# Kernel optimization log

Hardware: AMD Instinct MI355X
Metric: run time of the kernel (lower is better)

## Reference

```python
import jax, jax.numpy as jnp
import numpy as np

NBITS = 8
REDUCE = 64
OUT = 512


def setup_inputs() -> dict:
    key = jax.random.key(0)
    ks = jax.random.split(key, 6)
    T, B, C = 512, 16, 512
    ne = 2 ** NBITS
    x = jax.random.normal(ks[0], (T, B, C), dtype=jnp.float32)
    key_in = jax.random.normal(ks[1], (T, B, C), dtype=jnp.float32)  # unused by forward (overwritten)
    # xavier-ish init scales
    map_w = jax.random.normal(ks[2], (NBITS, C), dtype=jnp.float32) * np.sqrt(2.0 / (C + NBITS))
    map_b = jnp.zeros((NBITS,), dtype=jnp.float32)
    pw_w1 = jax.random.normal(ks[3], (REDUCE, C), dtype=jnp.float32) * np.sqrt(2.0 / (C + REDUCE))
    pw_w21 = jax.random.normal(ks[4], (ne, OUT * REDUCE), dtype=jnp.float32) * np.sqrt(2.0 / (ne + OUT * REDUCE))
    pw_w22 = jax.random.normal(ks[5], (ne, OUT * REDUCE), dtype=jnp.float32) * np.sqrt(2.0 / (ne + OUT * REDUCE))
    pw_B = jnp.zeros((1, 1, OUT), dtype=jnp.float32)
    return {"x": x, "key": key_in, "map_w": map_w, "map_b": map_b,
            "pw_w1": pw_w1, "pw_w21": pw_w21, "pw_w22": pw_w22, "pw_B": pw_B}


def reference(x, key, map_w, map_b, pw_w1, pw_w21, pw_w22, pw_B):
    # x: (T,B,C). `key` arg is overwritten by x in the original source.
    T, B, C = x.shape
    nbits = map_w.shape[0]
    out_dim = pw_B.shape[-1]
    reduce_dim = pw_w1.shape[0]

    k = x.reshape(T * B, C) @ map_w.T + map_b          # (T*B, nbits)
    z = jnp.clip(1.2 * jax.nn.sigmoid(k) - 0.1, 0.0, 1.0)  # saturated sigmoid
    code = (z > 0.5).astype(z.dtype)                   # eval: hard binary code

    pows = (2 ** jnp.arange(nbits, dtype=jnp.int32))   # bit_to_int weights
    qz1 = jnp.sum(code.astype(jnp.int32) * pows, axis=-1)          # (T*B,)
    qz2 = jnp.sum((1 - code.astype(jnp.int32)) * pows, axis=-1)    # (T*B,)

    # gather per-token expert rows and synthesize per-token weight matrix
    w2 = (pw_w21[qz1] + pw_w22[qz2]).reshape(T, B, out_dim, reduce_dim)

    # original computes (w2 @ pw_w1) @ x; reassociated as w2 @ (pw_w1 @ x)
    # to avoid materializing the (T,B,out,in) intermediate (same math)
    v = jnp.einsum('ri,tbi->tbr', pw_w1, x)            # (T,B,reduce)
    y = jnp.einsum('tbor,tbr->tbo', w2, v) + pw_B      # (T,B,out)

    loss = jnp.zeros((1,), dtype=x.dtype)
    return (y, loss)
```

## Files before the change

### kernel.cpp

```cpp
#include <hip/hip_runtime.h>

#define NTOK 8192
#define CDIM 512
#define NB   8
#define RD   64
#define OD   512

#define TPB_A 16
#define XPAD  4
#define XROW  (CDIM + XPAD)
#define XROW4 (XROW / 4)

typedef unsigned char u8;

__device__ __forceinline__ float4 f4add(float4 a, float4 b) {
    return make_float4(a.x + b.x, a.y + b.y, a.z + b.z, a.w + b.w);
}
__device__ __forceinline__ float dot4(float4 a, float4 b) {
    return a.x * b.x + a.y * b.y + a.z * b.z + a.w * b.w;
}

__global__ __launch_bounds__(128, 2) void phaseA(
    const float* __restrict__ x, const float* __restrict__ map_w,
    const float* __restrict__ map_b, const float* __restrict__ w1,
    u8* __restrict__ q_out, float* __restrict__ v_out,
    float* __restrict__ loss_out)
{
    const int t    = threadIdx.x;
    const int tok0 = blockIdx.x * TPB_A;
    __shared__ __align__(16) float xs[TPB_A * XROW];

    const float4* xsrc = (const float4*)(x + (size_t)tok0 * CDIM);
    #pragma unroll
    for (int i = t; i < TPB_A * (CDIM / 4); i += 128) {
        int r = i >> 7, c = i & 127;
        *((float4*)(xs + r * XROW) + c) = xsrc[i];
    }
    __syncthreads();

    {
        const int bit = t & 7, tk = t >> 3;
        const float4* m4 = (const float4*)(map_w + (size_t)bit * CDIM);
        const float4* x4 = (const float4*)xs + tk * XROW4;
        double a0 = 0.0, a1 = 0.0;
        for (int j = 0; j < CDIM / 4; ++j) {
            float4 m = m4[j], xv = x4[j];
            a0 += (double)m.x * (double)xv.x + (double)m.y * (double)xv.y;
            a1 += (double)m.z * (double)xv.z + (double)m.w * (double)xv.w;
        }
        double k = a0 + a1 + (double)map_b[bit];
        unsigned long long m = __ballot(k > 0.0);
        const int lane = t & 63;
        if ((lane & 7) == 0) {
            int g = lane >> 3;
            q_out[tok0 + tk] = (u8)((m >> (g * 8)) & 0xFFull);
        }
    }

    {
        const int r  = t & 63;
        const int tg = t >> 6;
        const float4* w4 = (const float4*)(w1 + (size_t)r * CDIM);
        const float4* xq = (const float4*)xs + (size_t)(tg * 8) * XROW4;
        float acc0 = 0.f, acc1 = 0.f, acc2 = 0.f, acc3 = 0.f;
        float acc4 = 0.f, acc5 = 0.f, acc6 = 0.f, acc7 = 0.f;

#define CONSUME(WV, J) { const int jj = (J);                       \
        acc0 += dot4(WV, xq[jj]);                                  \
        acc1 += dot4(WV, xq[1 * XROW4 + jj]);                      \
        acc2 += dot4(WV, xq[2 * XROW4 + jj]);                      \
        acc3 += dot4(WV, xq[3 * XROW4 + jj]);                      \
        acc4 += dot4(WV, xq[4 * XROW4 + jj]);                      \
        acc5 += dot4(WV, xq[5 * XROW4 + jj]);                      \
        acc6 += dot4(WV, xq[6 * XROW4 + jj]);                      \
        acc7 += dot4(WV, xq[7 * XROW4 + jj]); }

        float4 A0 = w4[0], A1 = w4[1], A2 = w4[2], A3 = w4[3];
        float4 B0, B1, B2, B3;
        for (int b = 0; b < CDIM / 4; b += 8) {
            B0 = w4[b + 4]; B1 = w4[b + 5]; B2 = w4[b + 6]; B3 = w4[b + 7];
            CONSUME(A0, b)     CONSUME(A1, b + 1)
            CONSUME(A2, b + 2) CONSUME(A3, b + 3)
            if (b + 8 < CDIM / 4) {
                A0 = w4[b + 8]; A1 = w4[b + 9]; A2 = w4[b + 10]; A3 = w4[b + 11];
            }
            CONSUME(B0, b + 4) CONSUME(B1, b + 5)
            CONSUME(B2, b + 6) CONSUME(B3, b + 7)
        }
#undef CONSUME

        float* vo = v_out + (size_t)(tok0 + tg * 8) * RD + r;
        vo[0 * RD] = acc0; vo[1 * RD] = acc1; vo[2 * RD] = acc2; vo[3 * RD] = acc3;
        vo[4 * RD] = acc4; vo[5 * RD] = acc5; vo[6 * RD] = acc6; vo[7 * RD] = acc7;
    }

    if (blockIdx.x == 0 && t == 0) loss_out[0] = 0.0f;
}

__global__ __launch_bounds__(128, 2) void phaseB(
    const u8* __restrict__ q_arr, const float* __restrict__ v_arr,
    const float* __restrict__ w21, const float* __restrict__ w22,
    const float* __restrict__ pwB, float* __restrict__ y)
{
    const int q  = blockIdx.x >> 2;
    const int qu = blockIdx.x & 3;
    const int t  = threadIdx.x;
    const int o  = qu * 128 + t;

    __shared__ unsigned short list[NTOK];
    __shared__ int cnt;
    __shared__ __align__(16) float vs[8 * RD];

    const uint4* qa = (const uint4*)q_arr;
    uint4 qv0 = qa[t], qv1 = qa[t + 128], qv2 = qa[t + 256], qv3 = qa[t + 384];

    const float4* pa = (const float4*)w21 + (size_t)q * (OD * RD / 4) + (size_t)o * (RD / 4);
    const float4* pb = (const float4*)w22 + (size_t)(255 - q) * (OD * RD / 4) + (size_t)o * (RD / 4);
    float4 a0 = pa[0],  a1 = pa[1],  a2 = pa[2],  a3 = pa[3],
           a4 = pa[4],  a5 = pa[5],  a6 = pa[6],  a7 = pa[7],
           a8 = pa[8],  a9 = pa[9],  a10 = pa[10], a11 = pa[11],
           a12 = pa[12], a13 = pa[13], a14 = pa[14], a15 = pa[15];
    float4 b0 = pb[0],  b1 = pb[1],  b2 = pb[2],  b3 = pb[3],
           b4 = pb[4],  b5 = pb[5],  b6 = pb[6],  b7 = pb[7],
           b8 = pb[8],  b9 = pb[9],  b10 = pb[10], b11 = pb[11],
           b12 = pb[12], b13 = pb[13], b14 = pb[14], b15 = pb[15];

    if (t == 0) cnt = 0;
    __syncthreads();

#define CHK(WORD, SB, OFF) { unsigned uw = (WORD); \
    if ((int)(uw & 0xFFu)         == q) list[atomicAdd(&cnt, 1)] = (unsigned short)((SB) + (OFF));     \
    if ((int)((uw >> 8)  & 0xFFu) == q) list[atomicAdd(&cnt, 1)] = (unsigned short)((SB) + (OFF) + 1); \
    if ((int)((uw >> 16) & 0xFFu) == q) list[atomicAdd(&cnt, 1)] = (unsigned short)((SB) + (OFF) + 2); \
    if ((int)(uw >> 24)           == q) list[atomicAdd(&cnt, 1)] = (unsigned short)((SB) + (OFF) + 3); }
    { int sb = t * 16;          CHK(qv0.x, sb, 0) CHK(qv0.y, sb, 4) CHK(qv0.z, sb, 8) CHK(qv0.w, sb, 12) }
    { int sb = (t + 128) * 16;  CHK(qv1.x, sb, 0) CHK(qv1.y, sb, 4) CHK(qv1.z, sb, 8) CHK(qv1.w, sb, 12) }
    { int sb = (t + 256) * 16;  CHK(qv2.x, sb, 0) CHK(qv2.y, sb, 4) CHK(qv2.z, sb, 8) CHK(qv2.w, sb, 12) }
    { int sb = (t + 384) * 16;  CHK(qv3.x, sb, 0) CHK(qv3.y, sb, 4) CHK(qv3.z, sb, 8) CHK(qv3.w, sb, 12) }
#undef CHK
    __syncthreads();
    const int n = cnt;
    if (n == 0) return;

    float4 w0 = f4add(a0, b0),  w1 = f4add(a1, b1),  w2 = f4add(a2, b2),  w3 = f4add(a3, b3),
           w4 = f4add(a4, b4),  w5 = f4add(a5, b5),  w6 = f4add(a6, b6),  w7 = f4add(a7, b7),
           w8 = f4add(a8, b8),  w9 = f4add(a9, b9),  w10 = f4add(a10, b10), w11 = f4add(a11, b11),
           w12 = f4add(a12, b12), w13 = f4add(a13, b13), w14 = f4add(a14, b14), w15 = f4add(a15, b15);
    const float bias = pwB[o];

    const float4* v4 = (const float4*)v_arr;
    for (int base = 0; base < n; base += 8) {
        const int nb = min(8, n - base);
        if (t < nb * 16)
            ((float4*)vs)[t] = v4[(size_t)list[base + (t >> 4)] * (RD / 4) + (t & 15)];
        __syncthreads();
        int i = 0;
        for (; i + 2 <= nb; i += 2) {
            const float4* p0 = (const float4*)vs + (size_t)i * 16;
            const float4* p1 = p0 + 16;
            float acc0 = bias, acc1 = bias;
#define STEP(J, W) { float4 u0 = p0[J], u1 = p1[J]; \
            acc0 += W.x * u0.x + W.y * u0.y + W.z * u0.z + W.w * u0.w; \
            acc1 += W.x * u1.x + W.y * u1.y + W.z * u1.z + W.w * u1.w; }
            STEP(0, w0)  STEP(1, w1)  STEP(2, w2)  STEP(3, w3)
            STEP(4, w4)  STEP(5, w5)  STEP(6, w6)  STEP(7, w7)
            STEP(8, w8)  STEP(9, w9)  STEP(10, w10) STEP(11, w11)
            STEP(12, w12) STEP(13, w13) STEP(14, w14) STEP(15, w15)
#undef STEP
            y[(size_t)list[base + i]     * OD + o] = acc0;
            y[(size_t)list[base + i + 1] * OD + o] = acc1;
        }
        if (i < nb) {
            const float4* p0 = (const float4*)vs + (size_t)i * 16;
            float acc0 = bias;
#define STEP1(J, W) { float4 u0 = p0[J]; \
            acc0 += W.x * u0.x + W.y * u0.y + W.z * u0.z + W.w * u0.w; }
            STEP1(0, w0)  STEP1(1, w1)  STEP1(2, w2)  STEP1(3, w3)
            STEP1(4, w4)  STEP1(5, w5)  STEP1(6, w6)  STEP1(7, w7)
            STEP1(8, w8)  STEP1(9, w9)  STEP1(10, w10) STEP1(11, w11)
            STEP1(12, w12) STEP1(13, w13) STEP1(14, w14) STEP1(15, w15)
#undef STEP1
            y[(size_t)list[base + i] * OD + o] = acc0;
        }
        __syncthreads();
    }
}

__global__ __launch_bounds__(256) void mono(
    const float* __restrict__ x, const float* __restrict__ map_w,
    const float* __restrict__ map_b, const float* __restrict__ w1,
    const float* __restrict__ w21, const float* __restrict__ w22,
    const float* __restrict__ pwB, float* __restrict__ y)
{
    const int tok = blockIdx.x;
    const int t   = threadIdx.x;
    __shared__ float xsh[CDIM];
    __shared__ float vsh[RD];
    __shared__ int qsh;

    if (t == 0) qsh = 0;
    for (int i = t; i < CDIM; i += 256) xsh[i] = x[(size_t)tok * CDIM + i];
    __syncthreads();

    if (t < NB) {
        double a = 0.0;
        const float* mrow = map_w + (size_t)t * CDIM;
        for (int j = 0; j < CDIM; ++j) a += (double)mrow[j] * (double)xsh[j];
        a += (double)map_b[t];
        if (a > 0.0) atomicOr(&qsh, 1 << t);
    }
    if (t < RD) {
        const float* wrow = w1 + (size_t)t * CDIM;
        float acc = 0.f;
        for (int j = 0; j < CDIM; ++j) acc += wrow[j] * xsh[j];
        vsh[t] = acc;
    }
    __syncthreads();

    const int q = qsh;
    for (int o = t; o < OD; o += 256) {
        const float* pa = w21 + (size_t)q * (OD * RD) + (size_t)o * RD;
        const float* pb = w22 + (size_t)(255 - q) * (OD * RD) + (size_t)o * RD;
        float acc = pwB[o];
        for (int r = 0; r < RD; ++r) acc += (pa[r] + pb[r]) * vsh[r];
        y[(size_t)tok * OD + o] = acc;
    }
    if (tok == 0 && t == 0) y[(size_t)NTOK * OD] = 0.0f;
}

extern "C" void kernel_launch(void* const* d_in, const int* in_sizes, int n_in,
                              void* d_out, int out_size, void* d_ws, size_t ws_size,
                              hipStream_t stream) {
    const float* x     = (const float*)d_in[0];
    const float* map_w = (const float*)d_in[2];
    const float* map_b = (const float*)d_in[3];
    const float* w1    = (const float*)d_in[4];
    const float* w21   = (const float*)d_in[5];
    const float* w22   = (const float*)d_in[6];
    const float* pwB   = (const float*)d_in[7];
    float* out = (float*)d_out;

    const size_t need = (size_t)NTOK + (size_t)NTOK * RD * sizeof(float);
    if (ws_size >= need) {
        u8*    q_ws = (u8*)d_ws;
        float* v_ws = (float*)((char*)d_ws + NTOK);
        phaseA<<<NTOK / TPB_A, 128, 0, stream>>>(x, map_w, map_b, w1, q_ws, v_ws,
                                                 out + (size_t)NTOK * OD);
        phaseB<<<256 * 4, 128, 0, stream>>>(q_ws, v_ws, w21, w22, pwB, out);
    } else {
        mono<<<NTOK, 256, 0, stream>>>(x, map_w, map_b, w1, w21, w22, pwB, out);
    }
}
```

Measured before the change: 198.1 us.

## Coalesce weight loads via LDS staging in both phase kernels

In phaseA, w1 is no longer read per thread along strided rows. It is loaded cooperatively in coalesced slices into a double-buffered shared-memory tile, with register prefetch of the next slice. In phaseB, the expert rows from w21/w22 are now read with fully coalesced, thread-contiguous float4 loads, summed, written to a rotated (bank-conflict-avoiding) shared buffer, and then read back per output row. This targets uncoalesced global access, at the cost of extra LDS usage, a barrier per slice, and lower occupancy from the larger shared footprint.

Result: slower. 206.7 us (+4.4%).

```diff
diff --git a/kernel.cpp b/kernel.cpp
--- a/kernel.cpp
+++ b/kernel.cpp
@@ -10,6 +10,8 @@
 #define XPAD  4
 #define XROW  (CDIM + XPAD)
 #define XROW4 (XROW / 4)
+#define SL    8
+#define NSL   (CDIM / 4 / SL)
 
 typedef unsigned char u8;
 
@@ -28,7 +30,8 @@
 {
     const int t    = threadIdx.x;
     const int tok0 = blockIdx.x * TPB_A;
-    __shared__ __align__(16) float xs[TPB_A * XROW];
+    __shared__ __align__(16) float  xs[TPB_A * XROW];
+    __shared__ __align__(16) float4 wsl[2][SL * RD];
 
     const float4* xsrc = (const float4*)(x + (size_t)tok0 * CDIM);
     #pragma unroll
@@ -36,6 +39,18 @@
         int r = i >> 7, c = i & 127;
         *((float4*)(xs + r * XROW) + c) = xsrc[i];
     }
+
+    const float4* w1g = (const float4*)w1;
+    const int i1 = 128 + t, i2 = 256 + t, i3 = 384 + t;
+    const int r0 = t  >> 3, c0 = t  & 7;
+    const int r1 = i1 >> 3, c1 = i1 & 7;
+    const int r2 = i2 >> 3, c2 = i2 & 7;
+    const int r3 = i3 >> 3, c3 = i3 & 7;
+    float4 A0 = w1g[r0 * 128 + c0];
+    float4 A1 = w1g[r1 * 128 + c1];
+    float4 A2 = w1g[r2 * 128 + c2];
+    float4 A3 = w1g[r3 * 128 + c3];
+
     __syncthreads();
 
     {
@@ -60,34 +75,40 @@
     {
         const int r  = t & 63;
         const int tg = t >> 6;
-        const float4* w4 = (const float4*)(w1 + (size_t)r * CDIM);
-        const float4* xq = (const float4*)xs + (size_t)(tg * 8) * XROW4;
+        const float4* xq4 = (const float4*)xs + (size_t)(tg * 8) * XROW4;
         float acc0 = 0.f, acc1 = 0.f, acc2 = 0.f, acc3 = 0.f;
         float acc4 = 0.f, acc5 = 0.f, acc6 = 0.f, acc7 = 0.f;
-
-#define CONSUME(WV, J) { const int jj = (J);                       \
-        acc0 += dot4(WV, xq[jj]);                                  \
-        acc1 += dot4(WV, xq[1 * XROW4 + jj]);                      \
-        acc2 += dot4(WV, xq[2 * XROW4 + jj]);                      \
-        acc3 += dot4(WV, xq[3 * XROW4 + jj]);                      \
-        acc4 += dot4(WV, xq[4 * XROW4 + jj]);                      \
-        acc5 += dot4(WV, xq[5 * XROW4 + jj]);                      \
-        acc6 += dot4(WV, xq[6 * XROW4 + jj]);                      \
-        acc7 += dot4(WV, xq[7 * XROW4 + jj]); }
-
-        float4 A0 = w4[0], A1 = w4[1], A2 = w4[2], A3 = w4[3];
         float4 B0, B1, B2, B3;
-        for (int b = 0; b < CDIM / 4; b += 8) {
-            B0 = w4[b + 4]; B1 = w4[b + 5]; B2 = w4[b + 6]; B3 = w4[b + 7];
-            CONSUME(A0, b)     CONSUME(A1, b + 1)
-            CONSUME(A2, b + 2) CONSUME(A3, b + 3)
-            if (b + 8 < CDIM / 4) {
-                A0 = w4[b + 8]; A1 = w4[b + 9]; A2 = w4[b + 10]; A3 = w4[b + 11];
+
+        for (int s = 0; s < NSL; ++s) {
+            float4* wb = &wsl[s & 1][0];
+            wb[c0 * RD + r0] = A0;
+            wb[c1 * RD + r1] = A1;
+            wb[c2 * RD + r2] = A2;
+            wb[c3 * RD + r3] = A3;
+            if (s + 1 < NSL) {
+                const int off = (s + 1) * SL;
+                B0 = w1g[r0 * 128 + off + c0];
+                B1 = w1g[r1 * 128 + off + c1];
+                B2 = w1g[r2 * 128 + off + c2];
+                B3 = w1g[r3 * 128 + off + c3];
             }
-            CONSUME(B0, b + 4) CONSUME(B1, b + 5)
-            CONSUME(B2, b + 6) CONSUME(B3, b + 7)
-        }
-#undef CONSUME
+            __syncthreads();
+            #pragma unroll
+            for (int i4 = 0; i4 < SL; ++i4) {
+                float4 wv = wb[i4 * RD + r];
+                const int jg = s * SL + i4;
+                acc0 += dot4(wv, xq4[jg]);
+                acc1 += dot4(wv, xq4[1 * XROW4 + jg]);
+                acc2 += dot4(wv, xq4[2 * XROW4 + jg]);
+                acc3 += dot4(wv, xq4[3 * XROW4 + jg]);
+                acc4 += dot4(wv, xq4[4 * XROW4 + jg]);
+                acc5 += dot4(wv, xq4[5 * XROW4 + jg]);
+                acc6 += dot4(wv, xq4[6 * XROW4 + jg]);
+                acc7 += dot4(wv, xq4[7 * XROW4 + jg]);
+            }
+            A0 = B0; A1 = B1; A2 = B2; A3 = B3;
+        }
 
         float* vo = v_out + (size_t)(tok0 + tg * 8) * RD + r;
         vo[0 * RD] = acc0; vo[1 * RD] = acc1; vo[2 * RD] = acc2; vo[3 * RD] = acc3;
@@ -109,21 +130,22 @@
 
     __shared__ unsigned short list[NTOK];
     __shared__ int cnt;
+    __shared__ __align__(16) float4 wsum[128 * 16];
     __shared__ __align__(16) float vs[8 * RD];
 
     const uint4* qa = (const uint4*)q_arr;
     uint4 qv0 = qa[t], qv1 = qa[t + 128], qv2 = qa[t + 256], qv3 = qa[t + 384];
 
-    const float4* pa = (const float4*)w21 + (size_t)q * (OD * RD / 4) + (size_t)o * (RD / 4);
-    const float4* pb = (const float4*)w22 + (size_t)(255 - q) * (OD * RD / 4) + (size_t)o * (RD / 4);
-    float4 a0 = pa[0],  a1 = pa[1],  a2 = pa[2],  a3 = pa[3],
-           a4 = pa[4],  a5 = pa[5],  a6 = pa[6],  a7 = pa[7],
-           a8 = pa[8],  a9 = pa[9],  a10 = pa[10], a11 = pa[11],
-           a12 = pa[12], a13 = pa[13], a14 = pa[14], a15 = pa[15];
-    float4 b0 = pb[0],  b1 = pb[1],  b2 = pb[2],  b3 = pb[3],
-           b4 = pb[4],  b5 = pb[5],  b6 = pb[6],  b7 = pb[7],
-           b8 = pb[8],  b9 = pb[9],  b10 = pb[10], b11 = pb[11],
-           b12 = pb[12], b13 = pb[13], b14 = pb[14], b15 = pb[15];
+    const float4* b21 = (const float4*)w21 + (size_t)q * (OD * RD / 4) + (size_t)qu * 2048;
+    const float4* b22 = (const float4*)w22 + (size_t)(255 - q) * (OD * RD / 4) + (size_t)qu * 2048;
+    float4 s0 = b21[t],        s1 = b21[t + 128],  s2 = b21[t + 256],  s3 = b21[t + 384],
+           s4 = b21[t + 512],  s5 = b21[t + 640],  s6 = b21[t + 768],  s7 = b21[t + 896],
+           s8 = b21[t + 1024], s9 = b21[t + 1152], s10 = b21[t + 1280], s11 = b21[t + 1408],
+           s12 = b21[t + 1536], s13 = b21[t + 1664], s14 = b21[t + 1792], s15 = b21[t + 1920];
+    float4 u0 = b22[t],        u1 = b22[t + 128],  u2 = b22[t + 256],  u3 = b22[t + 384],
+           u4 = b22[t + 512],  u5 = b22[t + 640],  u6 = b22[t + 768],  u7 = b22[t + 896],
+           u8 = b22[t + 1024], u9 = b22[t + 1152], u10 = b22[t + 1280], u11 = b22[t + 1408],
+           u12 = b22[t + 1536], u13 = b22[t + 1664], u14 = b22[t + 1792], u15 = b22[t + 1920];
 
     if (t == 0) cnt = 0;
     __syncthreads();
@@ -138,14 +160,28 @@
     { int sb = (t + 256) * 16;  CHK(qv2.x, sb, 0) CHK(qv2.y, sb, 4) CHK(qv2.z, sb, 8) CHK(qv2.w, sb, 12) }
     { int sb = (t + 384) * 16;  CHK(qv3.x, sb, 0) CHK(qv3.y, sb, 4) CHK(qv3.z, sb, 8) CHK(qv3.w, sb, 12) }
 #undef CHK
+
+#define PUT(K, SV, UV) { const int i = (K) * 128 + t; \
+    const int slot = (i & ~15) | (((i & 15) + (i >> 4)) & 15); \
+    wsum[slot] = f4add(SV, UV); }
+    PUT(0, s0, u0)   PUT(1, s1, u1)   PUT(2, s2, u2)   PUT(3, s3, u3)
+    PUT(4, s4, u4)   PUT(5, s5, u5)   PUT(6, s6, u6)   PUT(7, s7, u7)
+    PUT(8, s8, u8)   PUT(9, s9, u9)   PUT(10, s10, u10) PUT(11, s11, u11)
+    PUT(12, s12, u12) PUT(13, s13, u13) PUT(14, s14, u14) PUT(15, s15, u15)
+#undef PUT
     __syncthreads();
     const int n = cnt;
     if (n == 0) return;
 
-    float4 w0 = f4add(a0, b0),  w1 = f4add(a1, b1),  w2 = f4add(a2, b2),  w3 = f4add(a3, b3),
-           w4 = f4add(a4, b4),  w5 = f4add(a5, b5),  w6 = f4add(a6, b6),  w7 = f4add(a7, b7),
-           w8 = f4add(a8, b8),  w9 = f4add(a9, b9),  w10 = f4add(a10, b10), w11 = f4add(a11, b11),
-           w12 = f4add(a12, b12), w13 = f4add(a13, b13), w14 = f4add(a14, b14), w15 = f4add(a15, b15);
+    const int ss = t * 16;
+    float4 w0 = wsum[ss + ((0 + t) & 15)],  w1 = wsum[ss + ((1 + t) & 15)],
+           w2 = wsum[ss + ((2 + t) & 15)],  w3 = wsum[ss + ((3 + t) & 15)],
+           w4 = wsum[ss + ((4 + t) & 15)],  w5 = wsum[ss + ((5 + t) & 15)],
+           w6 = wsum[ss + ((6 + t) & 15)],  w7 = wsum[ss + ((7 + t) & 15)],
+           w8 = wsum[ss + ((8 + t) & 15)],  w9 = wsum[ss + ((9 + t) & 15)],
+           w10 = wsum[ss + ((10 + t) & 15)], w11 = wsum[ss + ((11 + t) & 15)],
+           w12 = wsum[ss + ((12 + t) & 15)], w13 = wsum[ss + ((13 + t) & 15)],
+           w14 = wsum[ss + ((14 + t) & 15)], w15 = wsum[ss + ((15 + t) & 15)];
     const float bias = pwB[o];
 
     const float4* v4 = (const float4*)v_arr;
@@ -159,9 +195,9 @@
             const float4* p0 = (const float4*)vs + (size_t)i * 16;
             const float4* p1 = p0 + 16;
             float acc0 = bias, acc1 = bias;
-#define STEP(J, W) { float4 u0 = p0[J], u1 = p1[J]; \
-            acc0 += W.x * u0.x + W.y * u0.y + W.z * u0.z + W.w * u0.w; \
-            acc1 += W.x * u1.x + W.y * u1.y + W.z * u1.z + W.w * u1.w; }
+#define STEP(J, W) { float4 x0 = p0[J], x1 = p1[J]; \
+            acc0 += W.x * x0.x + W.y * x0.y + W.z * x0.z + W.w * x0.w; \
+            acc1 += W.x * x1.x + W.y * x1.y + W.z * x1.z + W.w * x1.w; }
             STEP(0, w0)  STEP(1, w1)  STEP(2, w2)  STEP(3, w3)
             STEP(4, w4)  STEP(5, w5)  STEP(6, w6)  STEP(7, w7)
             STEP(8, w8)  STEP(9, w9)  STEP(10, w10) STEP(11, w11)
@@ -173,8 +209,8 @@
         if (i < nb) {
             const float4* p0 = (const float4*)vs + (size_t)i * 16;
             float acc0 = bias;
-#define STEP1(J, W) { float4 u0 = p0[J]; \
-            acc0 += W.x * u0.x + W.y * u0.y + W.z * u0.z + W.w * u0.w; }
+#define STEP1(J, W) { float4 x0 = p0[J]; \
+            acc0 += W.x * x0.x + W.y * x0.y + W.z * x0.z + W.w * x0.w; }
             STEP1(0, w0)  STEP1(1, w1)  STEP1(2, w2)  STEP1(3, w3)
             STEP1(4, w4)  STEP1(5, w5)  STEP1(6, w6)  STEP1(7, w7)
             STEP1(8, w8)  STEP1(9, w9)  STEP1(10, w10) STEP1(11, w11)
```

## Stage w1 slices through double-buffered LDS and read x via uniform scalar loads

Applied to the files above, without the earlier changes.

The v = w1·x projection in phaseA now stages w1 in 16-column slices, transposed into a double-buffered LDS tile with padded stride, and prefetches the next slice into registers while the current one is consumed. The x rows are read straight from global memory at wave-uniform addresses (readfirstlane), so they can become scalar/broadcast loads instead of LDS reads. The aim is to remove the per-thread strided global reads of w1 and LDS bandwidth pressure on x. In exchange it adds 8 barriers per block, more LDS use that may lower occupancy, and relies on x reads being cached.

Result: no change. 196.1 us (-1.0%).

```diff
diff --git a/kernel.cpp b/kernel.cpp
--- a/kernel.cpp
+++ b/kernel.cpp
@@ -10,6 +10,9 @@
 #define XPAD  4
 #define XROW  (CDIM + XPAD)
 #define XROW4 (XROW / 4)
+#define SLJ   16
+#define NSLICE (128 / SLJ)
+#define WSTR  65
 
 typedef unsigned char u8;
 
@@ -28,7 +31,8 @@
 {
     const int t    = threadIdx.x;
     const int tok0 = blockIdx.x * TPB_A;
-    __shared__ __align__(16) float xs[TPB_A * XROW];
+    __shared__ __align__(16) float  xs[TPB_A * XROW];
+    __shared__ __align__(16) float4 wt[2][SLJ * WSTR];
 
     const float4* xsrc = (const float4*)(x + (size_t)tok0 * CDIM);
     #pragma unroll
@@ -36,6 +40,15 @@
         int r = i >> 7, c = i & 127;
         *((float4*)(xs + r * XROW) + c) = xsrc[i];
     }
+
+    const float4* w1g = (const float4*)w1;
+    const int cc = t & 15;
+    const int rr = t >> 4;
+    const float4* wgb = w1g + rr * 128 + cc;
+    float4 P0 = wgb[0 * 1024], P1 = wgb[1 * 1024], P2 = wgb[2 * 1024],
+           P3 = wgb[3 * 1024], P4 = wgb[4 * 1024], P5 = wgb[5 * 1024],
+           P6 = wgb[6 * 1024], P7 = wgb[7 * 1024];
+
     __syncthreads();
 
     {
@@ -58,36 +71,51 @@
     }
 
     {
-        const int r  = t & 63;
-        const int tg = t >> 6;
-        const float4* w4 = (const float4*)(w1 + (size_t)r * CDIM);
-        const float4* xq = (const float4*)xs + (size_t)(tg * 8) * XROW4;
+        const int r   = t & 63;
+        const int tg  = t >> 6;
+        const int tgu = __builtin_amdgcn_readfirstlane(tg);
+        const float* xb = x + (size_t)(tok0 + tgu * 8) * CDIM;
+        const float4* xr0 = (const float4*)(xb + 0 * CDIM);
+        const float4* xr1 = (const float4*)(xb + 1 * CDIM);
+        const float4* xr2 = (const float4*)(xb + 2 * CDIM);
+        const float4* xr3 = (const float4*)(xb + 3 * CDIM);
+        const float4* xr4 = (const float4*)(xb + 4 * CDIM);
+        const float4* xr5 = (const float4*)(xb + 5 * CDIM);
+        const float4* xr6 = (const float4*)(xb + 6 * CDIM);
+        const float4* xr7 = (const float4*)(xb + 7 * CDIM);
         float acc0 = 0.f, acc1 = 0.f, acc2 = 0.f, acc3 = 0.f;
         float acc4 = 0.f, acc5 = 0.f, acc6 = 0.f, acc7 = 0.f;
 
-#define CONSUME(WV, J) { const int jj = (J);                       \
-        acc0 += dot4(WV, xq[jj]);                                  \
-        acc1 += dot4(WV, xq[1 * XROW4 + jj]);                      \
-        acc2 += dot4(WV, xq[2 * XROW4 + jj]);                      \
-        acc3 += dot4(WV, xq[3 * XROW4 + jj]);                      \
-        acc4 += dot4(WV, xq[4 * XROW4 + jj]);                      \
-        acc5 += dot4(WV, xq[5 * XROW4 + jj]);                      \
-        acc6 += dot4(WV, xq[6 * XROW4 + jj]);                      \
-        acc7 += dot4(WV, xq[7 * XROW4 + jj]); }
-
-        float4 A0 = w4[0], A1 = w4[1], A2 = w4[2], A3 = w4[3];
-        float4 B0, B1, B2, B3;
-        for (int b = 0; b < CDIM / 4; b += 8) {
-            B0 = w4[b + 4]; B1 = w4[b + 5]; B2 = w4[b + 6]; B3 = w4[b + 7];
-            CONSUME(A0, b)     CONSUME(A1, b + 1)
-            CONSUME(A2, b + 2) CONSUME(A3, b + 3)
-            if (b + 8 < CDIM / 4) {
-                A0 = w4[b + 8]; A1 = w4[b + 9]; A2 = w4[b + 10]; A3 = w4[b + 11];
+        for (int s = 0; s < NSLICE; ++s) {
+            float4* wb = &wt[s & 1][0];
+            wb[cc * WSTR + 0 * 8 + rr] = P0;
+            wb[cc * WSTR + 1 * 8 + rr] = P1;
+            wb[cc * WSTR + 2 * 8 + rr] = P2;
+            wb[cc * WSTR + 3 * 8 + rr] = P3;
+            wb[cc * WSTR + 4 * 8 + rr] = P4;
+            wb[cc * WSTR + 5 * 8 + rr] = P5;
+            wb[cc * WSTR + 6 * 8 + rr] = P6;
+            wb[cc * WSTR + 7 * 8 + rr] = P7;
+            if (s + 1 < NSLICE) {
+                const int go = (s + 1) * SLJ;
+                P0 = wgb[0 * 1024 + go]; P1 = wgb[1 * 1024 + go];
+                P2 = wgb[2 * 1024 + go]; P3 = wgb[3 * 1024 + go];
+                P4 = wgb[4 * 1024 + go]; P5 = wgb[5 * 1024 + go];
+                P6 = wgb[6 * 1024 + go]; P7 = wgb[7 * 1024 + go];
             }
-            CONSUME(B0, b + 4) CONSUME(B1, b + 5)
-            CONSUME(B2, b + 6) CONSUME(B3, b + 7)
-        }
-#undef CONSUME
+            __syncthreads();
+            #pragma unroll
+            for (int jj = 0; jj < SLJ; ++jj) {
+                const int j4 = s * SLJ + jj;
+                float4 wv = wb[jj * WSTR + r];
+                float4 x0 = xr0[j4], x1 = xr1[j4], x2 = xr2[j4], x3 = xr3[j4];
+                float4 x4v = xr4[j4], x5 = xr5[j4], x6 = xr6[j4], x7 = xr7[j4];
+                acc0 += dot4(wv, x0);  acc1 += dot4(wv, x1);
+                acc2 += dot4(wv, x2);  acc3 += dot4(wv, x3);
+                acc4 += dot4(wv, x4v); acc5 += dot4(wv, x5);
+                acc6 += dot4(wv, x6);  acc7 += dot4(wv, x7);
+            }
+        }
 
         float* vo = v_out + (size_t)(tok0 + tg * 8) * RD + r;
         vo[0 * RD] = acc0; vo[1 * RD] = acc1; vo[2 * RD] = acc2; vo[3 * RD] = acc3;
```

## Fuse both phases into one persistent kernel with a global atomic barrier

Applied to the files above, without the earlier changes.

Merges the projection/code phase and the expert-gather GEMV phase into a single 512-block kernel of 256 threads. A grid-wide spin barrier on a workspace counter separates the two phases, so the second launch and its gap disappear, and the expert weight rows are loaded before the barrier to hide their latency. Each block now handles one expert and half of the output columns and stages 16 tokens of v at a time. The risks are a deadlock if not all 512 blocks are co-resident (only a guard counter breaks the spin), an extra memset, and lower occupancy from the larger shared-memory footprint.

Measured after the change: 250.9 us. +26.7%, slower.

```diff
diff --git a/kernel.cpp b/kernel.cpp
--- a/kernel.cpp
+++ b/kernel.cpp
@@ -6,6 +6,7 @@
 #define RD   64
 #define OD   512
 
+#define NBLK  512
 #define TPB_A 16
 #define XPAD  4
 #define XROW  (CDIM + XPAD)
@@ -20,25 +21,33 @@
     return a.x * b.x + a.y * b.y + a.z * b.z + a.w * b.w;
 }
 
-__global__ __launch_bounds__(128, 2) void phaseA(
+__global__ __launch_bounds__(256, 2) void fused(
     const float* __restrict__ x, const float* __restrict__ map_w,
     const float* __restrict__ map_b, const float* __restrict__ w1,
-    u8* __restrict__ q_out, float* __restrict__ v_out,
-    float* __restrict__ loss_out)
+    const float* __restrict__ w21, const float* __restrict__ w22,
+    const float* __restrict__ pwB,
+    u8* __restrict__ q_arr, float* __restrict__ v_arr,
+    float* __restrict__ y, float* __restrict__ loss_out,
+    int* __restrict__ bar)
 {
     const int t    = threadIdx.x;
-    const int tok0 = blockIdx.x * TPB_A;
+    const int bid  = blockIdx.x;
+    const int tok0 = bid * TPB_A;
+
     __shared__ __align__(16) float xs[TPB_A * XROW];
+    __shared__ unsigned short list[NTOK];
+    __shared__ __align__(16) float vs[16 * RD];
+    __shared__ int cnt;
 
     const float4* xsrc = (const float4*)(x + (size_t)tok0 * CDIM);
     #pragma unroll
-    for (int i = t; i < TPB_A * (CDIM / 4); i += 128) {
+    for (int i = t; i < TPB_A * (CDIM / 4); i += 256) {
         int r = i >> 7, c = i & 127;
         *((float4*)(xs + r * XROW) + c) = xsrc[i];
     }
     __syncthreads();
 
-    {
+    if (t < 128) {
         const int bit = t & 7, tk = t >> 3;
         const float4* m4 = (const float4*)(map_w + (size_t)bit * CDIM);
         const float4* x4 = (const float4*)xs + tk * XROW4;
@@ -53,7 +62,7 @@
         const int lane = t & 63;
         if ((lane & 7) == 0) {
             int g = lane >> 3;
-            q_out[tok0 + tk] = (u8)((m >> (g * 8)) & 0xFFull);
+            q_arr[tok0 + tk] = (u8)((m >> (g * 8)) & 0xFFull);
         }
     }
 
@@ -61,19 +70,14 @@
         const int r  = t & 63;
         const int tg = t >> 6;
         const float4* w4 = (const float4*)(w1 + (size_t)r * CDIM);
-        const float4* xq = (const float4*)xs + (size_t)(tg * 8) * XROW4;
+        const float4* xq = (const float4*)xs + (size_t)(tg * 4) * XROW4;
         float acc0 = 0.f, acc1 = 0.f, acc2 = 0.f, acc3 = 0.f;
-        float acc4 = 0.f, acc5 = 0.f, acc6 = 0.f, acc7 = 0.f;
 
 #define CONSUME(WV, J) { const int jj = (J);                       \
         acc0 += dot4(WV, xq[jj]);                                  \
         acc1 += dot4(WV, xq[1 * XROW4 + jj]);                      \
         acc2 += dot4(WV, xq[2 * XROW4 + jj]);                      \
-        acc3 += dot4(WV, xq[3 * XROW4 + jj]);                      \
-        acc4 += dot4(WV, xq[4 * XROW4 + jj]);                      \
-        acc5 += dot4(WV, xq[5 * XROW4 + jj]);                      \
-        acc6 += dot4(WV, xq[6 * XROW4 + jj]);                      \
-        acc7 += dot4(WV, xq[7 * XROW4 + jj]); }
+        acc3 += dot4(WV, xq[3 * XROW4 + jj]); }
 
         float4 A0 = w4[0], A1 = w4[1], A2 = w4[2], A3 = w4[3];
         float4 B0, B1, B2, B3;
@@ -89,31 +93,15 @@
         }
 #undef CONSUME
 
-        float* vo = v_out + (size_t)(tok0 + tg * 8) * RD + r;
+        float* vo = v_arr + (size_t)(tok0 + tg * 4) * RD + r;
         vo[0 * RD] = acc0; vo[1 * RD] = acc1; vo[2 * RD] = acc2; vo[3 * RD] = acc3;
-        vo[4 * RD] = acc4; vo[5 * RD] = acc5; vo[6 * RD] = acc6; vo[7 * RD] = acc7;
-    }
-
-    if (blockIdx.x == 0 && t == 0) loss_out[0] = 0.0f;
-}
-
-__global__ __launch_bounds__(128, 2) void phaseB(
-    const u8* __restrict__ q_arr, const float* __restrict__ v_arr,
-    const float* __restrict__ w21, const float* __restrict__ w22,
-    const float* __restrict__ pwB, float* __restrict__ y)
-{
-    const int q  = blockIdx.x >> 2;
-    const int qu = blockIdx.x & 3;
-    const int t  = threadIdx.x;
-    const int o  = qu * 128 + t;
-
-    __shared__ unsigned short list[NTOK];
-    __shared__ int cnt;
-    __shared__ __align__(16) float vs[8 * RD];
-
-    const uint4* qa = (const uint4*)q_arr;
-    uint4 qv0 = qa[t], qv1 = qa[t + 128], qv2 = qa[t + 256], qv3 = qa[t + 384];
-
+    }
+
+    if (bid == 0 && t == 0) loss_out[0] = 0.0f;
+
+    const int q    = bid >> 1;
+    const int half = bid & 1;
+    const int o    = half * 256 + t;
     const float4* pa = (const float4*)w21 + (size_t)q * (OD * RD / 4) + (size_t)o * (RD / 4);
     const float4* pb = (const float4*)w22 + (size_t)(255 - q) * (OD * RD / 4) + (size_t)o * (RD / 4);
     float4 a0 = pa[0],  a1 = pa[1],  a2 = pa[2],  a3 = pa[3],
@@ -124,33 +112,45 @@
            b4 = pb[4],  b5 = pb[5],  b6 = pb[6],  b7 = pb[7],
            b8 = pb[8],  b9 = pb[9],  b10 = pb[10], b11 = pb[11],
            b12 = pb[12], b13 = pb[13], b14 = pb[14], b15 = pb[15];
+    const float bias = pwB[o];
+
+    __syncthreads();
+    if (t == 0) {
+        __threadfence();
+        atomicAdd(bar, 1);
+        int guard = 0;
+        while (atomicAdd(bar, 0) < NBLK) {
+            __builtin_amdgcn_s_sleep(8);
+            if (++guard > (1 << 22)) break;
+        }
+        __threadfence();
+    }
+    __syncthreads();
 
     if (t == 0) cnt = 0;
     __syncthreads();
-
+    const uint4* qa = (const uint4*)q_arr;
+    uint4 qv0 = qa[t], qv1 = qa[t + 256];
 #define CHK(WORD, SB, OFF) { unsigned uw = (WORD); \
     if ((int)(uw & 0xFFu)         == q) list[atomicAdd(&cnt, 1)] = (unsigned short)((SB) + (OFF));     \
     if ((int)((uw >> 8)  & 0xFFu) == q) list[atomicAdd(&cnt, 1)] = (unsigned short)((SB) + (OFF) + 1); \
     if ((int)((uw >> 16) & 0xFFu) == q) list[atomicAdd(&cnt, 1)] = (unsigned short)((SB) + (OFF) + 2); \
     if ((int)(uw >> 24)           == q) list[atomicAdd(&cnt, 1)] = (unsigned short)((SB) + (OFF) + 3); }
     { int sb = t * 16;          CHK(qv0.x, sb, 0) CHK(qv0.y, sb, 4) CHK(qv0.z, sb, 8) CHK(qv0.w, sb, 12) }
-    { int sb = (t + 128) * 16;  CHK(qv1.x, sb, 0) CHK(qv1.y, sb, 4) CHK(qv1.z, sb, 8) CHK(qv1.w, sb, 12) }
-    { int sb = (t + 256) * 16;  CHK(qv2.x, sb, 0) CHK(qv2.y, sb, 4) CHK(qv2.z, sb, 8) CHK(qv2.w, sb, 12) }
-    { int sb = (t + 384) * 16;  CHK(qv3.x, sb, 0) CHK(qv3.y, sb, 4) CHK(qv3.z, sb, 8) CHK(qv3.w, sb, 12) }
+    { int sb = (t + 256) * 16;  CHK(qv1.x, sb, 0) CHK(qv1.y, sb, 4) CHK(qv1.z, sb, 8) CHK(qv1.w, sb, 12) }
 #undef CHK
     __syncthreads();
     const int n = cnt;
     if (n == 0) return;
 
-    float4 w0 = f4add(a0, b0),  w1 = f4add(a1, b1),  w2 = f4add(a2, b2),  w3 = f4add(a3, b3),
-           w4 = f4add(a4, b4),  w5 = f4add(a5, b5),  w6 = f4add(a6, b6),  w7 = f4add(a7, b7),
-           w8 = f4add(a8, b8),  w9 = f4add(a9, b9),  w10 = f4add(a10, b10), w11 = f4add(a11, b11),
-           w12 = f4add(a12, b12), w13 = f4add(a13, b13), w14 = f4add(a14, b14), w15 = f4add(a15, b15);
-    const float bias = pwB[o];
+    float4 f0 = f4add(a0, b0),  f1 = f4add(a1, b1),  f2 = f4add(a2, b2),  f3 = f4add(a3, b3),
+           f4 = f4add(a4, b4),  f5 = f4add(a5, b5),  f6 = f4add(a6, b6),  f7 = f4add(a7, b7),
+           f8 = f4add(a8, b8),  f9 = f4add(a9, b9),  f10 = f4add(a10, b10), f11 = f4add(a11, b11),
+           f12 = f4add(a12, b12), f13 = f4add(a13, b13), f14 = f4add(a14, b14), f15 = f4add(a15, b15);
 
     const float4* v4 = (const float4*)v_arr;
-    for (int base = 0; base < n; base += 8) {
-        const int nb = min(8, n - base);
+    for (int base = 0; base < n; base += 16) {
+        const int nb = min(16, n - base);
         if (t < nb * 16)
             ((float4*)vs)[t] = v4[(size_t)list[base + (t >> 4)] * (RD / 4) + (t & 15)];
         __syncthreads();
@@ -162,10 +162,10 @@
 #define STEP(J, W) { float4 u0 = p0[J], u1 = p1[J]; \
             acc0 += W.x * u0.x + W.y * u0.y + W.z * u0.z + W.w * u0.w; \
             acc1 += W.x * u1.x + W.y * u1.y + W.z * u1.z + W.w * u1.w; }
-            STEP(0, w0)  STEP(1, w1)  STEP(2, w2)  STEP(3, w3)
-            STEP(4, w4)  STEP(5, w5)  STEP(6, w6)  STEP(7, w7)
-            STEP(8, w8)  STEP(9, w9)  STEP(10, w10) STEP(11, w11)
-            STEP(12, w12) STEP(13, w13) STEP(14, w14) STEP(15, w15)
+            STEP(0, f0)  STEP(1, f1)  STEP(2, f2)  STEP(3, f3)
+            STEP(4, f4)  STEP(5, f5)  STEP(6, f6)  STEP(7, f7)
+            STEP(8, f8)  STEP(9, f9)  STEP(10, f10) STEP(11, f11)
+            STEP(12, f12) STEP(13, f13) STEP(14, f14) STEP(15, f15)
 #undef STEP
             y[(size_t)list[base + i]     * OD + o] = acc0;
             y[(size_t)list[base + i + 1] * OD + o] = acc1;
@@ -175,10 +175,10 @@
             float acc0 = bias;
 #define STEP1(J, W) { float4 u0 = p0[J]; \
             acc0 += W.x * u0.x + W.y * u0.y + W.z * u0.z + W.w * u0.w; }
-            STEP1(0, w0)  STEP1(1, w1)  STEP1(2, w2)  STEP1(3, w3)
-            STEP1(4, w4)  STEP1(5, w5)  STEP1(6, w6)  STEP1(7, w7)
-            STEP1(8, w8)  STEP1(9, w9)  STEP1(10, w10) STEP1(11, w11)
-            STEP1(12, w12) STEP1(13, w13) STEP1(14, w14) STEP1(15, w15)
+            STEP1(0, f0)  STEP1(1, f1)  STEP1(2, f2)  STEP1(3, f3)
+            STEP1(4, f4)  STEP1(5, f5)  STEP1(6, f6)  STEP1(7, f7)
+            STEP1(8, f8)  STEP1(9, f9)  STEP1(10, f10) STEP1(11, f11)
+            STEP1(12, f12) STEP1(13, f13) STEP1(14, f14) STEP1(15, f15)
 #undef STEP1
             y[(size_t)list[base + i] * OD + o] = acc0;
         }
@@ -240,13 +240,16 @@
     const float* pwB   = (const float*)d_in[7];
     float* out = (float*)d_out;
 
-    const size_t need = (size_t)NTOK + (size_t)NTOK * RD * sizeof(float);
+    const size_t vq_bytes = (size_t)NTOK + (size_t)NTOK * RD * sizeof(float);
+    const size_t need = vq_bytes + 64;
     if (ws_size >= need) {
         u8*    q_ws = (u8*)d_ws;
         float* v_ws = (float*)((char*)d_ws + NTOK);
-        phaseA<<<NTOK / TPB_A, 128, 0, stream>>>(x, map_w, map_b, w1, q_ws, v_ws,
-                                                 out + (size_t)NTOK * OD);
-        phaseB<<<256 * 4, 128, 0, stream>>>(q_ws, v_ws, w21, w22, pwB, out);
+        int*   bar  = (int*)((char*)d_ws + vq_bytes);
+        hipMemsetAsync(bar, 0, sizeof(int), stream);
+        fused<<<NBLK, 256, 0, stream>>>(x, map_w, map_b, w1, w21, w22, pwB,
+                                        q_ws, v_ws, out,
+                                        out + (size_t)NTOK * OD, bar);
     } else {
         mono<<<NTOK, 256, 0, stream>>>(x, map_w, map_b, w1, w21, w22, pwB, out);
     }
```
